# Optimization experiments

Hardware: AMD Instinct MI355X
Metric: run time of the kernel (lower is better)

The kernel has to match this reference:

```python
import jax, jax.numpy as jnp
import numpy as np

D_IN = 1024
D_OUT = 1024

def setup_inputs() -> dict:
    key = jax.random.key(0)
    k1, k2 = jax.random.split(key)
    x = jax.random.normal(k1, (4, 2048, D_IN), dtype=jnp.float32)
    # Keras 'uniform' initializer: U(-0.05, 0.05); kernel has 4 slices, only 0..2 used
    kernel = jax.random.uniform(k2, (4, D_IN, D_OUT), dtype=jnp.float32, minval=-0.05, maxval=0.05)
    return {"x": x, "kernel": kernel}

def reference(x, kernel):
    # QKV projections: x [b, s, d] @ kernel[i] [d, e]
    WQ = jnp.einsum('bsd,de->bse', x, kernel[0])
    WK = jnp.einsum('bsd,de->bse', x, kernel[1])
    WV = jnp.einsum('bsd,de->bse', x, kernel[2])
    scale = 1.0 / jnp.sqrt(jnp.asarray(D_OUT, dtype=WQ.dtype))
    QK = jnp.einsum('bqe,bke->bqk', WQ, WK) * scale  # [b, s, s]
    A = jax.nn.softmax(QK, axis=-1)
    return jnp.einsum('bqk,bke->bqe', A, WV)  # [b, s, e]
```

## Files before the change

kernel.cpp:

```cpp
#include <hip/hip_runtime.h>
#include <hip/hip_bf16.h>
#include <cstdio>

typedef __bf16  bf16x8 __attribute__((ext_vector_type(8)));
typedef float   f32x4  __attribute__((ext_vector_type(4)));
typedef unsigned short u16;
typedef u16     u16x8  __attribute__((ext_vector_type(8)));
typedef u16     u16x4  __attribute__((ext_vector_type(4)));


__device__ __forceinline__ void gld_lds16(const void* g, void* l) {
  __builtin_amdgcn_global_load_lds(
      (const __attribute__((address_space(1))) unsigned int*)g,
      (__attribute__((address_space(3))) unsigned int*)l,
      16, 0, 0);
}

__device__ __forceinline__ u16 f2bf(float f) {
  union { float f; unsigned int u; } c{f};
  unsigned int u = c.u;
  u += 0x7fffu + ((u >> 16) & 1u);
  return (u16)(u >> 16);
}

__device__ __forceinline__ float bf2f(u16 h) {
  union { unsigned int u; float f; } c{(unsigned int)h << 16};
  return c.f;
}


__global__ __launch_bounds__(256) void prep_kernel(const float* __restrict__ x,
                                                   u16* __restrict__ xbf,
                                                   const float* __restrict__ w,
                                                   u16* __restrict__ wt,
                                                   float* __restrict__ rs) {
  __shared__ float tile[32][33];
  const int bid = blockIdx.x;
  if (bid < 4096) {
    const int i = (bid * 256 + threadIdx.x) * 8;
    float4 a = *(const float4*)(x + i);
    float4 b = *(const float4*)(x + i + 4);
    u16x8 r;
    r[0] = f2bf(a.x); r[1] = f2bf(a.y); r[2] = f2bf(a.z); r[3] = f2bf(a.w);
    r[4] = f2bf(b.x); r[5] = f2bf(b.y); r[6] = f2bf(b.z); r[7] = f2bf(b.w);
    *(u16x8*)(xbf + i) = r;
  } else if (bid < 7168) {
    const int b2 = bid - 4096;
    const int s = b2 >> 10, r = b2 & 1023;
    const int e0 = (r & 31) * 32, d0 = (r >> 5) * 32;
    const int tx = threadIdx.x & 31, ty = threadIdx.x >> 5;
    const float* in = w + (size_t)s * 1048576;
#pragma unroll
    for (int j = 0; j < 4; ++j)
      tile[ty + j * 8][tx] = in[(size_t)(d0 + ty + j * 8) * 1024 + e0 + tx];
    __syncthreads();
    u16* o = wt + (size_t)s * 1048576;
#pragma unroll
    for (int j = 0; j < 4; ++j)
      o[(size_t)(e0 + ty + j * 8) * 1024 + d0 + tx] = f2bf(tile[tx][ty + j * 8]);
  } else {
    const float4 z = {0.f, 0.f, 0.f, 0.f};
#pragma unroll
    for (int j = 0; j < 8; ++j)
      ((float4*)rs)[threadIdx.x + j * 256] = z;
  }
}


enum { EPI_QKV = 0, EPI_QK = 1, EPI_PV = 2 };

template <int EPI>
__global__ __launch_bounds__(256)
void gemm_bt(const u16* __restrict__ A, const u16* __restrict__ B,
             void* __restrict__ Cv, int K, int lda, int ldb, int ldc,
             long sA, long sB, long sC,
             float* __restrict__ rowsum, u16* __restrict__ auxK, u16* __restrict__ auxV) {
  constexpr int LDS_U16 = (EPI == EPI_QKV) ? (128 * 136) : (128 * 128);
  __shared__ __align__(16) u16 lds[LDS_U16];
  u16* As = lds;
  u16* Bs = lds + 128 * 64;

  const int t = threadIdx.x;
  const int w = t >> 6, l = t & 63;
  const int bz = blockIdx.z;
  const u16* Ab = A + (long)bz * sA;
  const u16* Bb = B + (long)bz * sB;
  const int m0 = blockIdx.y * 128, n0 = blockIdx.x * 128;
  const int wm = w & 1, wn = w >> 1;
  const int lr = l & 15, lq = l >> 4;
  const int srow = l >> 3;
  const int scol = ((l & 7) ^ ((l >> 3) & 7)) * 8;
  const int rsw = l & 7;

  f32x4 acc[4][4] = {};

  for (int k0 = 0; k0 < K; k0 += 64) {
    __syncthreads();
#pragma unroll
    for (int c = 0; c < 4; ++c) {
      const int rb = (w * 4 + c) * 8;
      gld_lds16(Ab + (long)(m0 + rb + srow) * lda + k0 + scol, (void*)(As + rb * 64));
      gld_lds16(Bb + (long)(n0 + rb + srow) * ldb + k0 + scol, (void*)(Bs + rb * 64));
    }
    __syncthreads();
#pragma unroll
    for (int j = 0; j < 2; ++j) {
      bf16x8 af[4], bfr[4];
#pragma unroll
      for (int i = 0; i < 4; ++i) {
        const int ch = ((j * 4 + lq) ^ rsw) * 8;
        af[i]  = *(const bf16x8*)(As + (wm * 64 + i * 16 + lr) * 64 + ch);
        bfr[i] = *(const bf16x8*)(Bs + (wn * 64 + i * 16 + lr) * 64 + ch);
      }
#pragma unroll
      for (int mi = 0; mi < 4; ++mi)
#pragma unroll
        for (int ni = 0; ni < 4; ++ni)
          acc[mi][ni] = __builtin_amdgcn_mfma_f32_16x16x32_bf16(af[mi], bfr[ni], acc[mi][ni], 0, 0, 0);
    }
  }

  if (EPI == EPI_QKV && n0 >= 2048) {
    u16* tt = lds;
    __syncthreads();
#pragma unroll
    for (int mi = 0; mi < 4; ++mi) {
      const int row0 = wm * 64 + mi * 16 + lq * 4;
#pragma unroll
      for (int ni = 0; ni < 4; ++ni) {
        const int col = wn * 64 + ni * 16 + lr;
        u16x4 v4;
#pragma unroll
        for (int i = 0; i < 4; ++i) v4[i] = f2bf(acc[mi][ni][i]);
        *(u16x4*)(tt + col * 136 + row0) = v4;
      }
    }
    __syncthreads();
    const int e0 = n0 - 2048;
    const long bb = m0 >> 11;
    const int kbase = m0 & 2047;
    u16* vt_base = auxV + bb * 2097152;
#pragma unroll
    for (int q = 0; q < 8; ++q) {
      const int chunk = q * 256 + t;
      const int c = chunk >> 4, r0 = (chunk & 15) * 8;
      u16x8 v = *(const u16x8*)(tt + c * 136 + r0);
      *(u16x8*)(vt_base + (long)(e0 + c) * 2048 + kbase + r0) = v;
    }
    return;
  }

  u16* qkv_out = nullptr;
  int nl0 = 0;
  if (EPI == EPI_QKV) {
    qkv_out = (n0 < 1024) ? (u16*)Cv : auxK;
    nl0 = n0 & 1023;
  }

#pragma unroll
  for (int mi = 0; mi < 4; ++mi) {
#pragma unroll
    for (int i = 0; i < 4; ++i) {
      const int row = m0 + wm * 64 + mi * 16 + lq * 4 + i;
      float inv;
      if (EPI == EPI_PV) inv = 1.0f / rowsum[bz * 2048 + row];
      float rs = 0.f;
#pragma unroll
      for (int ni = 0; ni < 4; ++ni) {
        const float val = acc[mi][ni][i];
        if (EPI == EPI_QKV) {
          const int col_l = nl0 + wn * 64 + ni * 16 + lr;
          qkv_out[(long)row * 1024 + col_l] = f2bf(val);
        } else if (EPI == EPI_QK) {
          const int col = n0 + wn * 64 + ni * 16 + lr;
          const u16 h = f2bf(__expf(val * 0.03125f));
          ((u16*)Cv)[(long)bz * sC + (long)row * ldc + col] = h;
          rs += bf2f(h);
        } else {
          const int col = n0 + wn * 64 + ni * 16 + lr;
          ((float*)Cv)[(long)bz * sC + (long)row * ldc + col] = val * inv;
        }
      }
      if (EPI == EPI_QK) {
        rs += __shfl_xor(rs, 1, 64);
        rs += __shfl_xor(rs, 2, 64);
        rs += __shfl_xor(rs, 4, 64);
        rs += __shfl_xor(rs, 8, 64);
        if (lr == 0) atomicAdd(rowsum + bz * 2048 + row, rs);
      }
    }
  }
}


extern "C" void kernel_launch(void* const* d_in, const int* in_sizes, int n_in,
                              void* d_out, int out_size, void* d_ws, size_t ws_size,
                              hipStream_t stream) {
  (void)in_sizes; (void)n_in; (void)out_size;
  const float* x    = (const float*)d_in[0];
  const float* kern = (const float*)d_in[1];
  float* out = (float*)d_out;
  char* ws = (char*)d_ws;
  const size_t MB = 1024 * 1024;
  u16*   xbf  = (u16*)(ws);
  u16*   WT   = (u16*)(ws + 16 * MB);
  u16*   Qc   = (u16*)(ws + 22 * MB);
  u16*   Kc   = (u16*)(ws + 38 * MB);
  u16*   VT   = (u16*)(ws + 54 * MB);
  u16*   SP   = (u16*)(ws + 70 * MB);
  float* RS   = (float*)(ws + 102 * MB);
  if (ws_size < 102 * MB + 32768)
    fprintf(stderr, "WARNING: ws_size %zu too small\n", ws_size);

  prep_kernel<<<7169, 256, 0, stream>>>(x, xbf, kern, WT, RS);
  gemm_bt<EPI_QKV><<<dim3(24, 64, 1), 256, 0, stream>>>(
      xbf, WT, Qc, 1024, 1024, 1024, 1024, 0, 0, 0, nullptr, Kc, VT);
  gemm_bt<EPI_QK><<<dim3(16, 16, 4), 256, 0, stream>>>(
      Qc, Kc, SP, 1024, 1024, 1024, 2048,
      2048L * 1024, 2048L * 1024, 2048L * 2048, RS, nullptr, nullptr);
  gemm_bt<EPI_PV><<<dim3(8, 16, 4), 256, 0, stream>>>(
      SP, VT, out, 2048, 2048, 2048, 1024,
      2048L * 2048, 1024L * 2048, 2048L * 1024, RS, nullptr, nullptr);
}
```

Measured before the change: 255.7 us.

## Add 256x256-tile double-buffered GEMM kernel for QKV and QK stages

Introduces a new 512-thread GEMM kernel with 256x256 output tiles and double-buffered LDS. It issues global-to-LDS prefetches of the next K tile between MFMA phases and raises wave priority around the MFMA bursts. The QKV projection and QK^T stages now use it, which cuts operand traffic per FLOP and overlaps loads with compute. In exchange, each block needs 128KB of LDS and many accumulator registers, which limits occupancy. The QKV grid of 384 blocks also fills the CUs unevenly.

```diff
diff --git a/kernel.cpp b/kernel.cpp
--- a/kernel.cpp
+++ b/kernel.cpp
@@ -27,6 +27,8 @@
   union { unsigned int u; float f; } c{(unsigned int)h << 16};
   return c.f;
 }
+
+enum { EPI_QKV = 0, EPI_QK = 1, EPI_PV = 2 };
 
 
 __global__ __launch_bounds__(256) void prep_kernel(const float* __restrict__ x,
@@ -67,7 +69,230 @@
 }
 
 
-enum { EPI_QKV = 0, EPI_QK = 1, EPI_PV = 2 };
+__device__ __forceinline__ void stage_half(const u16* __restrict__ g, int ld, int k0,
+                                           u16* ldsb, int w, int l) {
+  const int srow = l >> 3;
+  const int scol = ((l & 7) ^ (srow & 7)) * 8;
+#pragma unroll
+  for (int q = 0; q < 2; ++q) {
+    const int r = w * 16 + q * 8;
+    gld_lds16(g + (long)(r + srow) * ld + k0 + scol, (void*)(ldsb + r * 64));
+  }
+}
+
+template <int EPI>
+__global__ __launch_bounds__(512, 2)
+void gemm256_bt(const u16* __restrict__ A, const u16* __restrict__ B,
+                void* __restrict__ Cv, int K, int lda, int ldb, int ldc,
+                long sA, long sB, long sC,
+                float* __restrict__ rowsum, u16* __restrict__ auxK, u16* __restrict__ auxV) {
+  __shared__ __align__(16) u16 lds[65536];
+
+  const int t = threadIdx.x;
+  const int w = t >> 6, l = t & 63;
+  const int wm = w >> 2, wn = w & 3;
+  const int lr = l & 15, lq = l >> 4;
+  const int rsw = l & 7;
+  const int bz = blockIdx.z;
+  const int m0 = blockIdx.y * 256, n0 = blockIdx.x * 256;
+  const u16* Ar = A + (long)bz * sA + (long)m0 * lda;
+  const u16* Br = B + (long)bz * sB + (long)n0 * ldb;
+
+  u16* curA = lds;
+  u16* curB = lds + 16384;
+  u16* nxtA = lds + 32768;
+  u16* nxtB = lds + 49152;
+
+  const int nt = K >> 6;
+
+  f32x4 acc[8][4] = {};
+
+  stage_half(Ar,             lda, 0, curA,        w, l);
+  stage_half(Br,             ldb, 0, curB,        w, l);
+  stage_half(Br + 128 * ldb, ldb, 0, curB + 8192, w, l);
+  stage_half(Ar + 128 * lda, lda, 0, curA + 8192, w, l);
+  asm volatile("s_waitcnt vmcnt(4)" ::: "memory");
+  if (nt > 1) {
+    stage_half(Ar,             lda, 64, nxtA,        w, l);
+    stage_half(Br,             ldb, 64, nxtB,        w, l);
+    stage_half(Br + 128 * ldb, ldb, 64, nxtB + 8192, w, l);
+    asm volatile("s_waitcnt vmcnt(6)" ::: "memory");
+  } else {
+    asm volatile("s_waitcnt vmcnt(0)" ::: "memory");
+  }
+  __builtin_amdgcn_s_barrier();
+
+  for (int tt = 0; tt < nt; ++tt) {
+    const int kc = tt << 6;
+    bf16x8 a0[4][2], a1[4][2], b0[2][2], b1[2][2];
+
+#pragma unroll
+    for (int mi = 0; mi < 4; ++mi)
+#pragma unroll
+      for (int j = 0; j < 2; ++j)
+        a0[mi][j] = *(const bf16x8*)(curA + (wm * 128 + mi * 16 + lr) * 64 +
+                                     (((j * 4 + lq) ^ rsw) * 8));
+#pragma unroll
+    for (int ni = 0; ni < 2; ++ni)
+#pragma unroll
+      for (int j = 0; j < 2; ++j)
+        b0[ni][j] = *(const bf16x8*)(curB + (wn * 64 + ni * 16 + lr) * 64 +
+                                     (((j * 4 + lq) ^ rsw) * 8));
+    if (tt + 1 < nt)
+      stage_half(Ar + 128 * lda, lda, kc + 64, nxtA + 8192, w, l);
+    __builtin_amdgcn_s_barrier();
+    asm volatile("s_waitcnt lgkmcnt(0)" ::: "memory");
+    __builtin_amdgcn_sched_barrier(0);
+    __builtin_amdgcn_s_setprio(1);
+#pragma unroll
+    for (int mi = 0; mi < 4; ++mi)
+#pragma unroll
+      for (int ni = 0; ni < 2; ++ni)
+#pragma unroll
+        for (int j = 0; j < 2; ++j)
+          acc[mi][ni] = __builtin_amdgcn_mfma_f32_16x16x32_bf16(a0[mi][j], b0[ni][j], acc[mi][ni], 0, 0, 0);
+    __builtin_amdgcn_s_setprio(0);
+    __builtin_amdgcn_s_barrier();
+
+#pragma unroll
+    for (int ni = 0; ni < 2; ++ni)
+#pragma unroll
+      for (int j = 0; j < 2; ++j)
+        b1[ni][j] = *(const bf16x8*)(curB + (wn * 64 + (ni + 2) * 16 + lr) * 64 +
+                                     (((j * 4 + lq) ^ rsw) * 8));
+    __builtin_amdgcn_s_barrier();
+    asm volatile("s_waitcnt lgkmcnt(0)" ::: "memory");
+    __builtin_amdgcn_sched_barrier(0);
+    __builtin_amdgcn_s_setprio(1);
+#pragma unroll
+    for (int mi = 0; mi < 4; ++mi)
+#pragma unroll
+      for (int ni = 0; ni < 2; ++ni)
+#pragma unroll
+        for (int j = 0; j < 2; ++j)
+          acc[mi][ni + 2] = __builtin_amdgcn_mfma_f32_16x16x32_bf16(a0[mi][j], b1[ni][j], acc[mi][ni + 2], 0, 0, 0);
+    __builtin_amdgcn_s_setprio(0);
+    __builtin_amdgcn_s_barrier();
+
+#pragma unroll
+    for (int mi = 0; mi < 4; ++mi)
+#pragma unroll
+      for (int j = 0; j < 2; ++j)
+        a1[mi][j] = *(const bf16x8*)(curA + (wm * 128 + (mi + 4) * 16 + lr) * 64 +
+                                     (((j * 4 + lq) ^ rsw) * 8));
+    if (tt + 2 < nt)
+      stage_half(Br, ldb, kc + 128, curB, w, l);
+    __builtin_amdgcn_s_barrier();
+    asm volatile("s_waitcnt lgkmcnt(0)" ::: "memory");
+    __builtin_amdgcn_sched_barrier(0);
+    __builtin_amdgcn_s_setprio(1);
+#pragma unroll
+    for (int mi = 0; mi < 4; ++mi)
+#pragma unroll
+      for (int ni = 0; ni < 2; ++ni)
+#pragma unroll
+        for (int j = 0; j < 2; ++j)
+          acc[mi + 4][ni + 2] = __builtin_amdgcn_mfma_f32_16x16x32_bf16(a1[mi][j], b1[ni][j], acc[mi + 4][ni + 2], 0, 0, 0);
+    __builtin_amdgcn_s_setprio(0);
+    __builtin_amdgcn_s_barrier();
+
+    if (tt + 2 < nt) {
+      stage_half(Br + 128 * ldb, ldb, kc + 128, curB + 8192, w, l);
+      stage_half(Ar,             lda, kc + 128, curA,        w, l);
+    }
+    __builtin_amdgcn_s_barrier();
+    __builtin_amdgcn_sched_barrier(0);
+    __builtin_amdgcn_s_setprio(1);
+#pragma unroll
+    for (int mi = 0; mi < 4; ++mi)
+#pragma unroll
+      for (int ni = 0; ni < 2; ++ni)
+#pragma unroll
+        for (int j = 0; j < 2; ++j)
+          acc[mi + 4][ni] = __builtin_amdgcn_mfma_f32_16x16x32_bf16(a1[mi][j], b0[ni][j], acc[mi + 4][ni], 0, 0, 0);
+    __builtin_amdgcn_s_setprio(0);
+    if (tt + 2 < nt)      asm volatile("s_waitcnt vmcnt(6)" ::: "memory");
+    else if (tt + 1 < nt) asm volatile("s_waitcnt vmcnt(0)" ::: "memory");
+    __builtin_amdgcn_s_barrier();
+
+    { u16* x_ = curA; curA = nxtA; nxtA = x_; }
+    { u16* y_ = curB; curB = nxtB; nxtB = y_; }
+  }
+
+  if (EPI == EPI_QK) {
+#pragma unroll
+    for (int mi = 0; mi < 8; ++mi) {
+#pragma unroll
+      for (int i = 0; i < 4; ++i) {
+        const int row = m0 + wm * 128 + mi * 16 + lq * 4 + i;
+        float rs = 0.f;
+#pragma unroll
+        for (int ni = 0; ni < 4; ++ni) {
+          const int col = n0 + wn * 64 + ni * 16 + lr;
+          const u16 h = f2bf(__expf(acc[mi][ni][i] * 0.03125f));
+          ((u16*)Cv)[(long)bz * sC + (long)row * ldc + col] = h;
+          rs += bf2f(h);
+        }
+        rs += __shfl_xor(rs, 1, 64);
+        rs += __shfl_xor(rs, 2, 64);
+        rs += __shfl_xor(rs, 4, 64);
+        rs += __shfl_xor(rs, 8, 64);
+        if (lr == 0) atomicAdd(rowsum + bz * 2048 + row, rs);
+      }
+    }
+    return;
+  }
+
+  if (EPI == EPI_QKV && n0 >= 2048) {
+    u16* tp = lds;
+    const int e0 = n0 - 2048;
+    const long bb = m0 >> 11;
+    const int kbase = m0 & 2047;
+    u16* vt_base = auxV + bb * 2097152;
+#pragma unroll
+    for (int h = 0; h < 2; ++h) {
+      __syncthreads();
+      if ((wn >> 1) == h) {
+        const int cb = (wn & 1) * 64;
+#pragma unroll
+        for (int mi = 0; mi < 8; ++mi) {
+          const int row0 = wm * 128 + mi * 16 + lq * 4;
+#pragma unroll
+          for (int ni = 0; ni < 4; ++ni) {
+            const int col = cb + ni * 16 + lr;
+            u16x4 v4;
+#pragma unroll
+            for (int i = 0; i < 4; ++i) v4[i] = f2bf(acc[mi][ni][i]);
+            *(u16x4*)(tp + col * 264 + row0) = v4;
+          }
+        }
+      }
+      __syncthreads();
+#pragma unroll
+      for (int q = 0; q < 8; ++q) {
+        const int chunk = q * 512 + t;
+        const int c = chunk >> 5, r0 = (chunk & 31) * 8;
+        u16x8 v = *(const u16x8*)(tp + c * 264 + r0);
+        *(u16x8*)(vt_base + (long)(e0 + h * 128 + c) * 2048 + kbase + r0) = v;
+      }
+    }
+    return;
+  }
+
+  u16* qkv_out = (n0 < 1024) ? (u16*)Cv : auxK;
+  const int nl0 = n0 & 1023;
+#pragma unroll
+  for (int mi = 0; mi < 8; ++mi) {
+#pragma unroll
+    for (int i = 0; i < 4; ++i) {
+      const int row = m0 + wm * 128 + mi * 16 + lq * 4 + i;
+#pragma unroll
+      for (int ni = 0; ni < 4; ++ni)
+        qkv_out[(long)row * 1024 + nl0 + wn * 64 + ni * 16 + lr] = f2bf(acc[mi][ni][i]);
+    }
+  }
+}
+
 
 template <int EPI>
 __global__ __launch_bounds__(256)
@@ -121,7 +346,7 @@
   }
 
   if (EPI == EPI_QKV && n0 >= 2048) {
-    u16* tt = lds;
+    u16* tp = lds;
     __syncthreads();
 #pragma unroll
     for (int mi = 0; mi < 4; ++mi) {
@@ -132,7 +357,7 @@
         u16x4 v4;
 #pragma unroll
         for (int i = 0; i < 4; ++i) v4[i] = f2bf(acc[mi][ni][i]);
-        *(u16x4*)(tt + col * 136 + row0) = v4;
+        *(u16x4*)(tp + col * 136 + row0) = v4;
       }
     }
     __syncthreads();
@@ -144,7 +369,7 @@
     for (int q = 0; q < 8; ++q) {
       const int chunk = q * 256 + t;
       const int c = chunk >> 4, r0 = (chunk & 15) * 8;
-      u16x8 v = *(const u16x8*)(tt + c * 136 + r0);
+      u16x8 v = *(const u16x8*)(tp + c * 136 + r0);
       *(u16x8*)(vt_base + (long)(e0 + c) * 2048 + kbase + r0) = v;
     }
     return;
@@ -213,9 +438,9 @@
     fprintf(stderr, "WARNING: ws_size %zu too small\n", ws_size);
 
   prep_kernel<<<7169, 256, 0, stream>>>(x, xbf, kern, WT, RS);
-  gemm_bt<EPI_QKV><<<dim3(24, 64, 1), 256, 0, stream>>>(
+  gemm256_bt<EPI_QKV><<<dim3(12, 32, 1), 512, 0, stream>>>(
       xbf, WT, Qc, 1024, 1024, 1024, 1024, 0, 0, 0, nullptr, Kc, VT);
-  gemm_bt<EPI_QK><<<dim3(16, 16, 4), 256, 0, stream>>>(
+  gemm256_bt<EPI_QK><<<dim3(8, 8, 4), 512, 0, stream>>>(
       Qc, Kc, SP, 1024, 1024, 1024, 2048,
       2048L * 1024, 2048L * 1024, 2048L * 2048, RS, nullptr, nullptr);
   gemm_bt<EPI_PV><<<dim3(8, 16, 4), 256, 0, stream>>>(
```

Result: faster. 243.4 us (-4.8%).
